# Kernel optimization log

Hardware: AMD Instinct MI355X
Metric: run time of the kernel (lower is better)

Reference implementation:

```python
import jax, jax.numpy as jnp
import numpy as np

B, NC, CH, HF, WF = 2, 6, 256, 32, 88
N, CIN = 100000, 128
VOXEL_SIZE = jnp.array([0.075, 0.075, 0.2], dtype=jnp.float32)
PC_MIN = jnp.array([-54.0, -54.0, -5.0], dtype=jnp.float32)
DOWNSAMPLE = 8.0
DMIN, DMAX = 1.0, 60.0


def setup_inputs() -> dict:
    key = jax.random.key(0)
    ks = jax.random.split(key, 12)
    # voxel coords: (batch, z, y, x), batch column sorted to match the
    # original per-batch-loop concatenation order
    b = jnp.repeat(jnp.arange(B, dtype=jnp.int32), N // B)
    x = jax.random.randint(ks[0], (N,), 0, 1440, dtype=jnp.int32)
    y = jax.random.randint(ks[1], (N,), 0, 1440, dtype=jnp.int32)
    z = jax.random.randint(ks[2], (N,), 0, 40, dtype=jnp.int32)
    voxel_coords = jnp.stack([b, z, y, x], axis=1)
    voxel_features = jax.random.normal(ks[3], (N, CIN), dtype=jnp.float32)
    img_feats = jax.random.normal(ks[4], (B, NC, CH, HF, WF), dtype=jnp.float32)
    # pinhole intrinsics for a 704x256 image
    K = jnp.array([[500.0, 0.0, 352.0], [0.0, 500.0, 128.0], [0.0, 0.0, 1.0]], dtype=jnp.float32)
    intrins = K + 0.01 * jax.random.normal(ks[5], (B, NC, 3, 3), dtype=jnp.float32)
    post_rots = 0.5 * jnp.eye(3, dtype=jnp.float32) + 0.001 * jax.random.normal(ks[6], (B, NC, 3, 3), dtype=jnp.float32)
    post_trans = 0.01 * jax.random.normal(ks[7], (B, NC, 3), dtype=jnp.float32)
    # bda: near-identity 4x4
    bda = jnp.tile(jnp.eye(4, dtype=jnp.float32), (B, 1, 1))
    bda = bda.at[:, :3, :3].add(0.01 * jax.random.normal(ks[8], (B, 3, 3), dtype=jnp.float32))
    bda = bda.at[:, :3, 3].set(0.1 * jax.random.normal(ks[9], (B, 3), dtype=jnp.float32))
    # lidar->cam: standard axis permutation (x->z) so depth is positive for half the scene
    R = jnp.array([[0.0, -1.0, 0.0], [0.0, 0.0, -1.0], [1.0, 0.0, 0.0]], dtype=jnp.float32)
    l2c = jnp.tile(jnp.eye(4, dtype=jnp.float32), (B, NC, 1, 1))
    l2c = l2c.at[..., :3, :3].set(R + 0.01 * jax.random.normal(ks[10], (B, NC, 3, 3), dtype=jnp.float32))
    l2c = l2c.at[..., :3, 3].set(0.1 * jax.random.normal(ks[11], (B, NC, 3), dtype=jnp.float32))
    W = 0.02 * jax.random.normal(jax.random.fold_in(key, 99), (CIN, CH), dtype=jnp.float32)
    return dict(voxel_features=voxel_features, voxel_coords=voxel_coords, img_feats=img_feats,
                intrins=intrins, post_rots=post_rots, post_trans=post_trans, bda=bda,
                lidar2cam=l2c, W=W)


def reference(voxel_features, voxel_coords, img_feats, intrins, post_rots, post_trans, bda, lidar2cam, W):
    bidx = voxel_coords[:, 0]
    # voxel index (x,y,z) -> metric lidar coords
    p = voxel_coords[:, jnp.array([3, 2, 1])].astype(jnp.float32) * VOXEL_SIZE + PC_MIN  # [N,3]
    # undo bda augmentation: (p - t) @ inv(R).T
    binv = jnp.linalg.inv(bda[:, :3, :3])  # [B,3,3]
    pcam = jnp.einsum('nj,nij->ni', p - bda[bidx, :3, 3], binv[bidx])  # [N,3]
    # lidar2img = cam2img @ lidar2cam.T (faithful to original, incl. full 4x4 transpose)
    cam2img = jnp.tile(jnp.eye(4, dtype=intrins.dtype), (B, NC, 1, 1)).at[..., :3, :3].set(intrins)
    L = cam2img @ jnp.swapaxes(lidar2cam, -1, -2)  # [B,NC,4,4]
    Lv = L[bidx]  # [N,NC,4,4]
    pimg = jnp.einsum('nj,ncij->nci', pcam, Lv[:, :, :3, :3]) + Lv[:, :, :3, 3]  # [N,NC,3]
    pimg = jnp.concatenate([pimg[..., :2] / pimg[..., 2:3], pimg[..., 2:3]], axis=-1)
    pimg = jnp.einsum('ncj,ncij->nci', pimg, post_rots[bidx]) + post_trans[bidx]
    # gather_img_feature: round/clip + masked gather, scatter into zeros == multiply by mask
    coor = jnp.round(pimg[..., :2] / DOWNSAMPLE)
    depth = pimg[..., 2]
    mask = ((coor[..., 0] >= 0) & (coor[..., 0] < WF) & (coor[..., 1] >= 0) & (coor[..., 1] < HF)
            & (depth < DMAX) & (depth >= DMIN))  # [N,NC]
    xi = jnp.clip(coor[..., 0].astype(jnp.int32), 0, WF - 1)
    yi = jnp.clip(coor[..., 1].astype(jnp.int32), 0, HF - 1)
    cams = jnp.arange(NC)[None, :]
    g = img_feats[bidx[:, None], cams, :, yi, xi]  # [N,NC,CH]
    g = g * mask[..., None].astype(g.dtype)
    # sum over cameras, then Linear(256 -> CIN, no bias)
    img_voxel = jnp.einsum('nc,oc->no', g.sum(axis=1), W)  # [N,CIN]
    out_feats = jnp.concatenate([voxel_features, img_voxel], axis=0)  # [2N,CIN]
    out_coords = jnp.concatenate([voxel_coords, voxel_coords], axis=0)  # [2N,4]
    return out_feats, out_coords
```

## Files before the change

kernel.cpp:

```cpp
#include <hip/hip_runtime.h>
#include <math.h>

#define BB   2
#define NCAM 6
#define CH   256
#define HF   32
#define WF   88
#define NV   100000
#define CIN  128
#define VPB  16

typedef __attribute__((ext_vector_type(8))) short short8;
typedef __attribute__((ext_vector_type(4))) float f32x4;

static __device__ inline short f2bf(float f) {
    union { float f; unsigned u; } v; v.f = f;
    unsigned r = (v.u + 0x7fffu + ((v.u >> 16) & 1u)) >> 16;
    return (short)r;
}
static __device__ inline float bflo(unsigned int pk) {
    union { unsigned int u; float f; } a; a.u = pk << 16; return a.f;
}
static __device__ inline float bfhi(unsigned int pk) {
    union { unsigned int u; float f; } a; a.u = pk & 0xffff0000u; return a.f;
}

__global__ void prep_params_w(const float* __restrict__ intrins,
                              const float* __restrict__ post_rots,
                              const float* __restrict__ post_trans,
                              const float* __restrict__ bda,
                              const float* __restrict__ l2c,
                              const float* __restrict__ W,
                              double* __restrict__ params,
                              short*  __restrict__ Wbf)
{
    if (blockIdx.x > 0) {
        int chunk = blockIdx.x - 1;
        int l = threadIdx.x;
        int nt = chunk >> 3, kk = chunk & 7;
        int n = nt * 16 + (l & 15);
        int k = kk * 32 + (l >> 4) * 8;
        short v[8];
        #pragma unroll
        for (int j = 0; j < 8; j++) v[j] = f2bf(W[n * CH + k + j]);
        *(short8*)(Wbf + ((size_t)chunk * 64 + l) * 8) = *(short8*)v;
        return;
    }

    int t = threadIdx.x;
    if (t >= BB * NCAM) return;
    int b = t / NCAM;

    const float* Bm = bda + b * 16;
    double a00 = Bm[0], a01 = Bm[1], a02 = Bm[2],  tx = Bm[3];
    double a10 = Bm[4], a11 = Bm[5], a12 = Bm[6],  ty = Bm[7];
    double a20 = Bm[8], a21 = Bm[9], a22 = Bm[10], tz = Bm[11];

    double det = a00*(a11*a22 - a12*a21) - a01*(a10*a22 - a12*a20) + a02*(a10*a21 - a11*a20);
    double id  = 1.0 / det;
    double inv[3][3];
    inv[0][0] =  (a11*a22 - a12*a21) * id;
    inv[0][1] = -(a01*a22 - a02*a21) * id;
    inv[0][2] =  (a01*a12 - a02*a11) * id;
    inv[1][0] = -(a10*a22 - a12*a20) * id;
    inv[1][1] =  (a00*a22 - a02*a20) * id;
    inv[1][2] = -(a00*a12 - a02*a10) * id;
    inv[2][0] =  (a10*a21 - a11*a20) * id;
    inv[2][1] = -(a00*a21 - a01*a20) * id;
    inv[2][2] =  (a00*a11 - a01*a10) * id;

    const float* In = intrins + t * 9;
    const float* Lc = l2c + t * 16;

    double M3[3][3];
    #pragma unroll
    for (int i = 0; i < 3; i++)
        #pragma unroll
        for (int j = 0; j < 3; j++)
            M3[i][j] = (double)In[i*3+0] * (double)Lc[j*4+0]
                     + (double)In[i*3+1] * (double)Lc[j*4+1]
                     + (double)In[i*3+2] * (double)Lc[j*4+2];

    double M[3][3];
    #pragma unroll
    for (int i = 0; i < 3; i++)
        #pragma unroll
        for (int j = 0; j < 3; j++)
            M[i][j] = M3[i][0]*inv[0][j] + M3[i][1]*inv[1][j] + M3[i][2]*inv[2][j];

    double* P = params + t * 24;
    #pragma unroll
    for (int i = 0; i < 3; i++)
        #pragma unroll
        for (int j = 0; j < 3; j++)
            P[i*3+j] = M[i][j];
    #pragma unroll
    for (int i = 0; i < 3; i++)
        P[9+i] = -(M[i][0]*tx + M[i][1]*ty + M[i][2]*tz);
    #pragma unroll
    for (int i = 0; i < 9; i++) P[12+i] = (double)post_rots[t*9 + i];
    #pragma unroll
    for (int i = 0; i < 3; i++) P[21+i] = (double)post_trans[t*3 + i];
}

__global__ __launch_bounds__(256) void transpose_img(const float* __restrict__ img,
                                                     unsigned short* __restrict__ imgT)
{
    __shared__ float tile[32][89];
    int bid = blockIdx.x;
    int cg  = bid & 7;
    int y   = (bid >> 3) & 31;
    int bc  = bid >> 8;
    int t   = threadIdx.x;

    const float* src = img + ((size_t)(bc * CH + cg * 32)) * (HF * WF) + y * WF;
    #pragma unroll
    for (int i = 0; i < 11; i++) {
        int lin = i * 256 + t;
        int ch  = lin / 88;
        int x   = lin - ch * 88;
        tile[ch][x] = src[(size_t)ch * (HF * WF) + x];
    }
    __syncthreads();

    unsigned short* dst = imgT + ((size_t)(bc * HF + y) * WF) * CH + cg * 32;
    #pragma unroll
    for (int j = 0; j < 6; j++) {
        int lin2 = j * 256 + t;
        if (j == 5 && t >= 128) break;
        int x  = lin2 >> 4;
        int cp = lin2 & 15;
        unsigned short lo = (unsigned short)f2bf(tile[2 * cp][x]);
        unsigned short hi = (unsigned short)f2bf(tile[2 * cp + 1][x]);
        unsigned int pk = (unsigned int)lo | ((unsigned int)hi << 16);
        *(unsigned int*)(dst + (size_t)x * CH + 2 * cp) = pk;
    }
}

struct POF { int o; float m; };

template <bool TRANS>
__global__ __launch_bounds__(256) void fused_gather_mm(
    const float*  __restrict__ vf,
    const int*    __restrict__ coords,
    const void*   __restrict__ imgv,
    const double* __restrict__ params,
    const short*  __restrict__ Wbf,
    float*        __restrict__ out)
{
    const int t  = threadIdx.x;
    const int n0 = blockIdx.x * VPB;

    {
        const float4* vf4 = (const float4*)vf;
        float4*       o4  = (float4*)out;
        int base = n0 * (CIN / 4);
        o4[base + t]       = vf4[base + t];
        o4[base + 256 + t] = vf4[base + 256 + t];
    }
    if (t < VPB * 4) {
        int gi = n0 * 4 + t;
        float cv = (float)coords[gi];
        const size_t cb = (size_t)2 * NV * CIN;
        out[cb + gi]                  = cv;
        out[cb + (size_t)NV * 4 + gi] = cv;
    }

    __shared__ POF pof[VPB][NCAM];
    __shared__ __align__(16) short aFrag[8 * 64 * 8];

    if (t < VPB * NCAM) {
        int vi = t / NCAM, c = t - vi * NCAM;
        int n  = n0 + vi;
        int b  = coords[n * 4 + 0];
        int zi = coords[n * 4 + 1];
        int yi = coords[n * 4 + 2];
        int xi = coords[n * 4 + 3];
        double px = (double)xi * (double)0.075f + (-54.0);
        double py = (double)yi * (double)0.075f + (-54.0);
        double pz = (double)zi * (double)0.2f   + (-5.0);
        const double* P = params + (b * NCAM + c) * 24;
        double X = P[0]*px + P[1]*py + P[2]*pz + P[9];
        double Y = P[3]*px + P[4]*py + P[5]*pz + P[10];
        double Z = P[6]*px + P[7]*py + P[8]*pz + P[11];
        double u = X / Z;
        double v = Y / Z;
        double q0 = P[12]*u + P[13]*v + P[14]*Z + P[21];
        double q1 = P[15]*u + P[16]*v + P[17]*Z + P[22];
        double q2 = P[18]*u + P[19]*v + P[20]*Z + P[23];
        double cx = rint(q0 * 0.125);
        double cy = rint(q1 * 0.125);
        bool m = (cx >= 0.0) && (cx < (double)WF) && (cy >= 0.0) && (cy < (double)HF)
              && (q2 < 60.0) && (q2 >= 1.0);
        int o = 0;
        if (m) {
            int ix = (int)cx, iy = (int)cy;
            if (TRANS) o = ((b * NCAM + c) * HF + iy) * WF + ix;
            else       o = (b * NCAM + c) * (CH * HF * WF) + iy * WF + ix;
        }
        POF p2; p2.o = o; p2.m = m ? 1.0f : 0.0f;
        pof[vi][c] = p2;
    }
    __syncthreads();

    {
        const int l  = t & 63;
        const int kk = t >> 6;
        const int vi = l & 15;
        const int k0 = kk * 32 + ((l >> 4) & 3) * 8;

        float g[16];
        #pragma unroll
        for (int j = 0; j < 16; j++) g[j] = 0.0f;

        if (TRANS) {
            const unsigned short* imgT = (const unsigned short*)imgv;
            #pragma unroll
            for (int c = 0; c < NCAM; c++) {
                POF p2 = pof[vi][c];
                float w = p2.m;
                const unsigned short* px = imgT + (size_t)p2.o * CH;
                uint4 A = *(const uint4*)(px + k0);
                uint4 B2 = *(const uint4*)(px + k0 + 128);
                g[0]  = fmaf(w, bflo(A.x),  g[0]);  g[1]  = fmaf(w, bfhi(A.x),  g[1]);
                g[2]  = fmaf(w, bflo(A.y),  g[2]);  g[3]  = fmaf(w, bfhi(A.y),  g[3]);
                g[4]  = fmaf(w, bflo(A.z),  g[4]);  g[5]  = fmaf(w, bfhi(A.z),  g[5]);
                g[6]  = fmaf(w, bflo(A.w),  g[6]);  g[7]  = fmaf(w, bfhi(A.w),  g[7]);
                g[8]  = fmaf(w, bflo(B2.x), g[8]);  g[9]  = fmaf(w, bfhi(B2.x), g[9]);
                g[10] = fmaf(w, bflo(B2.y), g[10]); g[11] = fmaf(w, bfhi(B2.y), g[11]);
                g[12] = fmaf(w, bflo(B2.z), g[12]); g[13] = fmaf(w, bfhi(B2.z), g[13]);
                g[14] = fmaf(w, bflo(B2.w), g[14]); g[15] = fmaf(w, bfhi(B2.w), g[15]);
            }
        } else {
            const float* img = (const float*)imgv;
            #pragma unroll
            for (int c = 0; c < NCAM; c++) {
                POF p2 = pof[vi][c];
                float w = p2.m;
                #pragma unroll
                for (int j = 0; j < 8; j++) {
                    g[j]     = fmaf(w, img[(size_t)(k0 + j)       * (HF * WF) + p2.o], g[j]);
                    g[8 + j] = fmaf(w, img[(size_t)(k0 + 128 + j) * (HF * WF) + p2.o], g[8 + j]);
                }
            }
        }

        short tmp[16];
        #pragma unroll
        for (int j = 0; j < 16; j++) tmp[j] = f2bf(g[j]);
        *(short8*)(aFrag + (kk * 64 + l) * 8)       = *(short8*)&tmp[0];
        *(short8*)(aFrag + ((kk + 4) * 64 + l) * 8) = *(short8*)&tmp[8];
    }
    __syncthreads();

    {
        const int w    = t >> 6;
        const int lane = t & 63;
        f32x4 acc0 = {0.f, 0.f, 0.f, 0.f};
        f32x4 acc1 = {0.f, 0.f, 0.f, 0.f};
        const short8* Bf = (const short8*)Wbf;
        #pragma unroll
        for (int kk = 0; kk < 8; kk++) {
            short8 a  = *(const short8*)(aFrag + (kk * 64 + lane) * 8);
            short8 b0 = Bf[((2 * w)     * 8 + kk) * 64 + lane];
            short8 b1 = Bf[((2 * w + 1) * 8 + kk) * 64 + lane];
            acc0 = __builtin_amdgcn_mfma_f32_16x16x32_bf16(a, b0, acc0, 0, 0, 0);
            acc1 = __builtin_amdgcn_mfma_f32_16x16x32_bf16(a, b1, acc1, 0, 0, 0);
        }
        float* oiv = out + (size_t)NV * CIN;
        int col = lane & 15, rq = lane >> 4;
        #pragma unroll
        for (int r = 0; r < 4; r++) {
            int n = n0 + rq * 4 + r;
            oiv[(size_t)n * CIN + (2 * w)     * 16 + col] = acc0[r];
            oiv[(size_t)n * CIN + (2 * w + 1) * 16 + col] = acc1[r];
        }
    }
}

extern "C" void kernel_launch(void* const* d_in, const int* in_sizes, int n_in,
                              void* d_out, int out_size, void* d_ws, size_t ws_size,
                              hipStream_t stream)
{
    const float* vf      = (const float*)d_in[0];
    const int*   coords  = (const int*)d_in[1];
    const float* img     = (const float*)d_in[2];
    const float* intrins = (const float*)d_in[3];
    const float* prots   = (const float*)d_in[4];
    const float* ptrans  = (const float*)d_in[5];
    const float* bda     = (const float*)d_in[6];
    const float* l2c     = (const float*)d_in[7];
    const float* W       = (const float*)d_in[8];
    float* out = (float*)d_out;

    double* params = (double*)d_ws;
    const size_t wbf_off  = 4096;
    const size_t wbf_sz   = (size_t)8 * 8 * 64 * 8 * sizeof(short);
    const size_t imgT_off = wbf_off + wbf_sz;
    const size_t needed   = imgT_off + (size_t)BB * NCAM * HF * WF * CH * sizeof(unsigned short);

    short* Wbf = (short*)((char*)d_ws + wbf_off);

    prep_params_w<<<65, 64, 0, stream>>>(intrins, prots, ptrans, bda, l2c, W, params, Wbf);

    if (ws_size >= needed) {
        unsigned short* imgT = (unsigned short*)((char*)d_ws + imgT_off);
        transpose_img<<<BB * NCAM * HF * 8, 256, 0, stream>>>(img, imgT);
        fused_gather_mm<true><<<NV / VPB, 256, 0, stream>>>(vf, coords, imgT, params, Wbf, out);
    } else {
        fused_gather_mm<false><<<NV / VPB, 256, 0, stream>>>(vf, coords, img, params, Wbf, out);
    }
}
```

Baseline: 222.1 us.

## Process 32 voxels per block to reuse W fragments across two MFMA row tiles

Doubles the voxels handled per block from 16 to 32 and reorganizes the gather so each wave collects four K-chunks for one 16-voxel tile. In the matmul, each wave now loads its W fragments once and applies them to two A tiles, halving W global reads per voxel. The number of blocks drops by half (3125), which reduces per-block overhead but also lowers parallelism and adds register and LDS use.

```diff
diff --git a/kernel.cpp b/kernel.cpp
--- a/kernel.cpp
+++ b/kernel.cpp
@@ -8,7 +8,7 @@
 #define WF   88
 #define NV   100000
 #define CIN  128
-#define VPB  16
+#define VPB  32
 
 typedef __attribute__((ext_vector_type(8))) short short8;
 typedef __attribute__((ext_vector_type(4))) float f32x4;
@@ -155,8 +155,9 @@
         const float4* vf4 = (const float4*)vf;
         float4*       o4  = (float4*)out;
         int base = n0 * (CIN / 4);
-        o4[base + t]       = vf4[base + t];
-        o4[base + 256 + t] = vf4[base + 256 + t];
+        #pragma unroll
+        for (int i = 0; i < 4; i++)
+            o4[base + i * 256 + t] = vf4[base + i * 256 + t];
     }
     if (t < VPB * 4) {
         int gi = n0 * 4 + t;
@@ -167,7 +168,7 @@
     }
 
     __shared__ POF pof[VPB][NCAM];
-    __shared__ __align__(16) short aFrag[8 * 64 * 8];
+    __shared__ __align__(16) short aFrag[16 * 64 * 8];
 
     if (t < VPB * NCAM) {
         int vi = t / NCAM, c = t - vi * NCAM;
@@ -204,76 +205,97 @@
     __syncthreads();
 
     {
-        const int l  = t & 63;
-        const int kk = t >> 6;
-        const int vi = l & 15;
-        const int k0 = kk * 32 + ((l >> 4) & 3) * 8;
-
-        float g[16];
-        #pragma unroll
-        for (int j = 0; j < 16; j++) g[j] = 0.0f;
+        const int l   = t & 63;
+        const int w   = t >> 6;
+        const int vt  = w >> 1;
+        const int kb  = (w & 1) * 4;
+        const int vi  = vt * 16 + (l & 15);
+        const int q   = l >> 4;
+
+        float g[4][8];
+        #pragma unroll
+        for (int i = 0; i < 4; i++)
+            #pragma unroll
+            for (int j = 0; j < 8; j++) g[i][j] = 0.0f;
 
         if (TRANS) {
             const unsigned short* imgT = (const unsigned short*)imgv;
             #pragma unroll
             for (int c = 0; c < NCAM; c++) {
                 POF p2 = pof[vi][c];
-                float w = p2.m;
-                const unsigned short* px = imgT + (size_t)p2.o * CH;
-                uint4 A = *(const uint4*)(px + k0);
-                uint4 B2 = *(const uint4*)(px + k0 + 128);
-                g[0]  = fmaf(w, bflo(A.x),  g[0]);  g[1]  = fmaf(w, bfhi(A.x),  g[1]);
-                g[2]  = fmaf(w, bflo(A.y),  g[2]);  g[3]  = fmaf(w, bfhi(A.y),  g[3]);
-                g[4]  = fmaf(w, bflo(A.z),  g[4]);  g[5]  = fmaf(w, bfhi(A.z),  g[5]);
-                g[6]  = fmaf(w, bflo(A.w),  g[6]);  g[7]  = fmaf(w, bfhi(A.w),  g[7]);
-                g[8]  = fmaf(w, bflo(B2.x), g[8]);  g[9]  = fmaf(w, bfhi(B2.x), g[9]);
-                g[10] = fmaf(w, bflo(B2.y), g[10]); g[11] = fmaf(w, bfhi(B2.y), g[11]);
-                g[12] = fmaf(w, bflo(B2.z), g[12]); g[13] = fmaf(w, bfhi(B2.z), g[13]);
-                g[14] = fmaf(w, bflo(B2.w), g[14]); g[15] = fmaf(w, bfhi(B2.w), g[15]);
+                float wm = p2.m;
+                const unsigned short* px = imgT + (size_t)p2.o * CH + q * 8;
+                #pragma unroll
+                for (int k2 = 0; k2 < 4; k2++) {
+                    uint4 A = *(const uint4*)(px + (kb + k2) * 32);
+                    g[k2][0] = fmaf(wm, bflo(A.x), g[k2][0]);
+                    g[k2][1] = fmaf(wm, bfhi(A.x), g[k2][1]);
+                    g[k2][2] = fmaf(wm, bflo(A.y), g[k2][2]);
+                    g[k2][3] = fmaf(wm, bfhi(A.y), g[k2][3]);
+                    g[k2][4] = fmaf(wm, bflo(A.z), g[k2][4]);
+                    g[k2][5] = fmaf(wm, bfhi(A.z), g[k2][5]);
+                    g[k2][6] = fmaf(wm, bflo(A.w), g[k2][6]);
+                    g[k2][7] = fmaf(wm, bfhi(A.w), g[k2][7]);
+                }
             }
         } else {
             const float* img = (const float*)imgv;
             #pragma unroll
             for (int c = 0; c < NCAM; c++) {
                 POF p2 = pof[vi][c];
-                float w = p2.m;
+                float wm = p2.m;
                 #pragma unroll
-                for (int j = 0; j < 8; j++) {
-                    g[j]     = fmaf(w, img[(size_t)(k0 + j)       * (HF * WF) + p2.o], g[j]);
-                    g[8 + j] = fmaf(w, img[(size_t)(k0 + 128 + j) * (HF * WF) + p2.o], g[8 + j]);
+                for (int k2 = 0; k2 < 4; k2++) {
+                    int k0 = (kb + k2) * 32 + q * 8;
+                    #pragma unroll
+                    for (int j = 0; j < 8; j++)
+                        g[k2][j] = fmaf(wm, img[(size_t)(k0 + j) * (HF * WF) + p2.o], g[k2][j]);
                 }
             }
         }
 
-        short tmp[16];
-        #pragma unroll
-        for (int j = 0; j < 16; j++) tmp[j] = f2bf(g[j]);
-        *(short8*)(aFrag + (kk * 64 + l) * 8)       = *(short8*)&tmp[0];
-        *(short8*)(aFrag + ((kk + 4) * 64 + l) * 8) = *(short8*)&tmp[8];
+        #pragma unroll
+        for (int k2 = 0; k2 < 4; k2++) {
+            short tmp[8];
+            #pragma unroll
+            for (int j = 0; j < 8; j++) tmp[j] = f2bf(g[k2][j]);
+            int chunk = vt * 8 + kb + k2;
+            *(short8*)(aFrag + (chunk * 64 + l) * 8) = *(short8*)tmp;
+        }
     }
     __syncthreads();
 
     {
         const int w    = t >> 6;
         const int lane = t & 63;
-        f32x4 acc0 = {0.f, 0.f, 0.f, 0.f};
-        f32x4 acc1 = {0.f, 0.f, 0.f, 0.f};
+        f32x4 acc[2][2];
+        #pragma unroll
+        for (int a2 = 0; a2 < 2; a2++)
+            #pragma unroll
+            for (int b2 = 0; b2 < 2; b2++)
+                acc[a2][b2] = (f32x4){0.f, 0.f, 0.f, 0.f};
         const short8* Bf = (const short8*)Wbf;
         #pragma unroll
         for (int kk = 0; kk < 8; kk++) {
-            short8 a  = *(const short8*)(aFrag + (kk * 64 + lane) * 8);
             short8 b0 = Bf[((2 * w)     * 8 + kk) * 64 + lane];
             short8 b1 = Bf[((2 * w + 1) * 8 + kk) * 64 + lane];
-            acc0 = __builtin_amdgcn_mfma_f32_16x16x32_bf16(a, b0, acc0, 0, 0, 0);
-            acc1 = __builtin_amdgcn_mfma_f32_16x16x32_bf16(a, b1, acc1, 0, 0, 0);
+            short8 a0 = *(const short8*)(aFrag + ((0 * 8 + kk) * 64 + lane) * 8);
+            short8 a1 = *(const short8*)(aFrag + ((1 * 8 + kk) * 64 + lane) * 8);
+            acc[0][0] = __builtin_amdgcn_mfma_f32_16x16x32_bf16(a0, b0, acc[0][0], 0, 0, 0);
+            acc[0][1] = __builtin_amdgcn_mfma_f32_16x16x32_bf16(a0, b1, acc[0][1], 0, 0, 0);
+            acc[1][0] = __builtin_amdgcn_mfma_f32_16x16x32_bf16(a1, b0, acc[1][0], 0, 0, 0);
+            acc[1][1] = __builtin_amdgcn_mfma_f32_16x16x32_bf16(a1, b1, acc[1][1], 0, 0, 0);
         }
         float* oiv = out + (size_t)NV * CIN;
         int col = lane & 15, rq = lane >> 4;
         #pragma unroll
-        for (int r = 0; r < 4; r++) {
-            int n = n0 + rq * 4 + r;
-            oiv[(size_t)n * CIN + (2 * w)     * 16 + col] = acc0[r];
-            oiv[(size_t)n * CIN + (2 * w + 1) * 16 + col] = acc1[r];
+        for (int a2 = 0; a2 < 2; a2++) {
+            #pragma unroll
+            for (int r = 0; r < 4; r++) {
+                int n = n0 + a2 * 16 + rq * 4 + r;
+                oiv[(size_t)n * CIN + (2 * w)     * 16 + col] = acc[a2][0][r];
+                oiv[(size_t)n * CIN + (2 * w + 1) * 16 + col] = acc[a2][1][r];
+            }
         }
     }
 }
```

After: 218.7 us. Within noise of the previous version (-1.5%).
